# Kernel optimization log

Hardware: AMD Instinct MI355X
Metric: run time of the kernel (lower is better)

## Reference

```python
import jax, jax.numpy as jnp
import numpy as np

BN_EPS = 1e-5
NN_CHUNK = 1024  # unknown points processed per distance-matrix tile


def _batch_ids(cnt, total):
    # contiguous per-batch layout -> batch id of each point via cumsum/searchsorted
    return jnp.searchsorted(jnp.cumsum(cnt), jnp.arange(total), side='right')


def three_nn(unknown, known, ub_id, kb_id):
    """Ragged brute-force 3-NN. Returns (squared dists [N,3], global idx [N,3])."""
    N = unknown.shape[0]
    nchunk = N // NN_CHUNK
    u = unknown.reshape(nchunk, NN_CHUNK, 3)
    ub = ub_id.reshape(nchunk, NN_CHUNK)

    def body(args):
        uc, bc = args
        d2 = jnp.sum((uc[:, None, :] - known[None, :, :]) ** 2, axis=-1)  # [chunk, M]
        d2 = jnp.where(bc[:, None] == kb_id[None, :], d2, jnp.inf)  # mask cross-batch pairs
        neg_d, idx = jax.lax.top_k(-d2, 3)
        return -neg_d, idx

    d2, idx = jax.lax.map(body, (u, ub))
    return d2.reshape(N, 3), idx.reshape(N, 3)


def three_interpolate(known_feats, idx, weight):
    # gather [N,3,C] then inverse-distance weighted sum -> [N,C]
    gathered = known_feats[idx]  # [N,3,C]
    return jnp.einsum('nkc,nk->nc', gathered, weight)


def conv_bn_relu(x, W, gamma, beta):
    # 1x1 Conv2d over [1,C,N,1] == pointwise matmul; BN (training stats) over points
    h = x @ W.T  # [N, C_out]
    mean = jnp.mean(h, axis=0)
    var = jnp.mean((h - mean) ** 2, axis=0)  # biased, as torch BN normalization
    h = (h - mean) * jax.lax.rsqrt(var + BN_EPS) * gamma + beta
    return jax.nn.relu(h)


def setup_inputs() -> dict:
    key = jax.random.key(0)
    ks = jax.random.split(key, 10)
    B, Nper, Mper, C1, C2 = 4, 16384, 4096, 128, 256
    N, M = B * Nper, B * Mper
    unknown = jax.random.normal(ks[0], (N, 3), jnp.float32) * 10.0
    known = jax.random.normal(ks[1], (M, 3), jnp.float32) * 10.0
    unknown_feats = jax.random.normal(ks[2], (N, C1), jnp.float32)
    known_feats = jax.random.normal(ks[3], (M, C2), jnp.float32)
    unknown_batch_cnt = jnp.full((B,), Nper, jnp.int32)
    known_batch_cnt = jnp.full((B,), Mper, jnp.int32)
    Cin = C1 + C2  # 384
    W1 = jax.random.normal(ks[4], (256, Cin), jnp.float32) * (1.0 / np.sqrt(Cin))
    W2 = jax.random.normal(ks[5], (256, 256), jnp.float32) * (1.0 / np.sqrt(256))
    g1 = jnp.ones((256,), jnp.float32); b1 = jnp.zeros((256,), jnp.float32)
    g2 = jnp.ones((256,), jnp.float32); b2 = jnp.zeros((256,), jnp.float32)
    return {"unknown": unknown, "unknown_batch_cnt": unknown_batch_cnt,
            "known": known, "known_batch_cnt": known_batch_cnt,
            "unknown_feats": unknown_feats, "known_feats": known_feats,
            "W1": W1, "g1": g1, "b1": b1, "W2": W2, "g2": g2, "b2": b2}


def reference(unknown, unknown_batch_cnt, known, known_batch_cnt,
              unknown_feats, known_feats, W1, g1, b1, W2, g2, b2):
    ub_id = _batch_ids(unknown_batch_cnt, unknown.shape[0])
    kb_id = _batch_ids(known_batch_cnt, known.shape[0])
    dist, idx = three_nn(unknown, known, ub_id, kb_id)  # squared dists, as CUDA kernel
    dist_recip = 1.0 / (dist + 1e-8)
    weight = dist_recip / jnp.sum(dist_recip, axis=-1, keepdims=True)
    interpolated = three_interpolate(known_feats, idx, weight)  # [N, C2]
    new_features = jnp.concatenate([interpolated, unknown_feats], axis=1)  # [N, C2+C1]
    new_features = conv_bn_relu(new_features, W1, g1, b1)
    new_features = conv_bn_relu(new_features, W2, g2, b2)
    return new_features  # [N, 256]
```

## Files before the change

kernel.cpp:

```cpp
#include <hip/hip_runtime.h>
#include <math.h>

typedef __attribute__((ext_vector_type(8))) short short8;
typedef __attribute__((ext_vector_type(4))) float f32x4;

#define INF 3.0e38f

__device__ __forceinline__ unsigned short f2bf(float x) {
    union { float f; unsigned u; } v; v.f = x;
    unsigned r = v.u + 0x7FFF + ((v.u >> 16) & 1);
    return (unsigned short)(r >> 16);
}

__global__ __launch_bounds__(256) void knn3_kernel(
    const float* __restrict__ unk, const float* __restrict__ kn,
    const int* __restrict__ ucnt, const int* __restrict__ kcnt,
    int B, int N, float* __restrict__ wgt, int* __restrict__ idxo)
{
    __shared__ float md[4][64][3];
    __shared__ float d2g[64];
    __shared__ unsigned long long mk[4][64][3];

    int tid = threadIdx.x;
    int s = __builtin_amdgcn_readfirstlane(tid >> 6);
    int lane = tid & 63;
    int pbase = blockIdx.x * 64;
    int p = pbase + lane;

    int cum = 0, bb = 0;
    for (int i = 0; i < B; i++) { int c = ucnt[i]; if (pbase >= cum) bb = i; cum += c; }
    int kstart = 0;
    for (int i = 0; i < bb; i++) kstart += kcnt[i];
    int kend = kstart + kcnt[bb];

    float ux = unk[p * 3 + 0], uy = unk[p * 3 + 1], uz = unk[p * 3 + 2];

    int qlen = (kend - kstart) >> 2;
    int jbase = kstart + s * qlen;
    const float* kq = kn + (size_t)jbase * 3;

    float d0 = INF, d1 = INF, d2 = INF;
    auto upd = [&](float e) {
        float m0 = fmaxf(e, d0);
        float m1 = fmaxf(e, d1);
        d0 = fminf(e, d0);
        d1 = fminf(m0, d1);
        d2 = fminf(m1, d2);
    };

    for (int i = 0; i < qlen; i += 8) {
        float e[8];
#pragma unroll
        for (int c = 0; c < 8; c++) {
            float kx = kq[(i + c) * 3 + 0];
            float ky = kq[(i + c) * 3 + 1];
            float kz = kq[(i + c) * 3 + 2];
            float dx = kx - ux, dy = ky - uy, dz = kz - uz;
            e[c] = __builtin_fmaf(dx, dx, __builtin_fmaf(dy, dy, dz * dz));
        }
#pragma unroll
        for (int c = 0; c < 8; c++) upd(e[c]);
    }

    md[s][lane][0] = d0; md[s][lane][1] = d1; md[s][lane][2] = d2;
    __syncthreads();
    if (tid < 64) {
        float v0 = INF, v1 = INF, v2 = INF;
#pragma unroll
        for (int w = 0; w < 4; w++)
#pragma unroll
            for (int k = 0; k < 3; k++) {
                float e = md[w][tid][k];
                float m0 = fmaxf(e, v0);
                float m1 = fmaxf(e, v1);
                v0 = fminf(e, v0);
                v1 = fminf(m0, v1);
                v2 = fminf(m1, v2);
            }
        d2g[tid] = v2;
    }
    __syncthreads();
    float thr = d2g[lane];

    unsigned long long s0 = ~0ULL, s1 = ~0ULL, s2 = ~0ULL;
    auto insK = [&](unsigned long long k) {
        bool c0 = k < s0;
        unsigned long long t0 = c0 ? k : s0;
        unsigned long long t1 = c0 ? s0 : k;
        bool c1 = t1 < s1;
        unsigned long long u0 = c1 ? t1 : s1;
        unsigned long long u1 = c1 ? s1 : t1;
        s0 = t0; s1 = u0;
        s2 = u1 < s2 ? u1 : s2;
    };
    auto mkkey = [](float e, int gj) {
        return ((unsigned long long)__float_as_uint(e) << 32) | (unsigned)gj;
    };

    for (int i = 0; i < qlen; i += 4) {
        float e[4];
#pragma unroll
        for (int c = 0; c < 4; c++) {
            float kx = kq[(i + c) * 3 + 0];
            float ky = kq[(i + c) * 3 + 1];
            float kz = kq[(i + c) * 3 + 2];
            float dx = kx - ux, dy = ky - uy, dz = kz - uz;
            e[c] = __builtin_fmaf(dx, dx, __builtin_fmaf(dy, dy, dz * dz));
        }
        float m4 = fminf(fminf(e[0], e[1]), fminf(e[2], e[3]));
        if (m4 <= thr) {
            int gj = jbase + i;
            insK(mkkey(e[0], gj + 0));
            insK(mkkey(e[1], gj + 1));
            insK(mkkey(e[2], gj + 2));
            insK(mkkey(e[3], gj + 3));
        }
    }

    mk[s][lane][0] = s0; mk[s][lane][1] = s1; mk[s][lane][2] = s2;
    __syncthreads();

    if (tid < 64) {
        s0 = s1 = s2 = ~0ULL;
#pragma unroll
        for (int qq = 0; qq < 4; qq++)
#pragma unroll
            for (int kk = 0; kk < 3; kk++)
                insK(mk[qq][tid][kk]);

        float dd0 = __uint_as_float((unsigned)(s0 >> 32));
        float dd1 = __uint_as_float((unsigned)(s1 >> 32));
        float dd2 = __uint_as_float((unsigned)(s2 >> 32));
        float r0 = 1.0f / (dd0 + 1e-8f);
        float r1 = 1.0f / (dd1 + 1e-8f);
        float r2 = 1.0f / (dd2 + 1e-8f);
        float rs = 1.0f / (r0 + r1 + r2);
        int pp = pbase + tid;
        wgt[pp * 3 + 0] = r0 * rs;
        wgt[pp * 3 + 1] = r1 * rs;
        wgt[pp * 3 + 2] = r2 * rs;
        idxo[pp * 3 + 0] = (int)(unsigned)s0;
        idxo[pp * 3 + 1] = (int)(unsigned)s1;
        idxo[pp * 3 + 2] = (int)(unsigned)s2;
    }
}

__global__ __launch_bounds__(256) void build_a1_kernel(
    const float* __restrict__ wgt, const int* __restrict__ idxv,
    const float* __restrict__ kfeat, const float* __restrict__ ufeat,
    unsigned short* __restrict__ A1, int N)
{
    int t = blockIdx.x * 256 + threadIdx.x;
    int p = t >> 6, c4 = t & 63;
    if (p >= N) return;
    float w0 = wgt[p * 3 + 0], w1 = wgt[p * 3 + 1], w2 = wgt[p * 3 + 2];
    int j0 = idxv[p * 3 + 0], j1 = idxv[p * 3 + 1], j2 = idxv[p * 3 + 2];
    float4 v0 = ((const float4*)(kfeat + (size_t)j0 * 256))[c4];
    float4 v1 = ((const float4*)(kfeat + (size_t)j1 * 256))[c4];
    float4 v2 = ((const float4*)(kfeat + (size_t)j2 * 256))[c4];
    ushort4 ob;
    ob.x = f2bf(v0.x * w0 + v1.x * w1 + v2.x * w2);
    ob.y = f2bf(v0.y * w0 + v1.y * w1 + v2.y * w2);
    ob.z = f2bf(v0.z * w0 + v1.z * w1 + v2.z * w2);
    ob.w = f2bf(v0.w * w0 + v1.w * w1 + v2.w * w2);
    *(ushort4*)(A1 + (size_t)p * 384 + c4 * 4) = ob;
    float2 u = ((const float2*)(ufeat + (size_t)p * 128))[c4];
    ushort2 ub; ub.x = f2bf(u.x); ub.y = f2bf(u.y);
    *(ushort2*)(A1 + (size_t)p * 384 + 256 + c4 * 2) = ub;
}

__global__ __launch_bounds__(256) void wconv_kernel(
    const float* __restrict__ W1, const float* __restrict__ W2,
    unsigned short* __restrict__ W1b, unsigned short* __restrict__ W2b,
    int n1, int n2)
{
    int i = blockIdx.x * 256 + threadIdx.x;
    if (i < n1) W1b[i] = f2bf(W1[i]);
    int j = i - n1;
    if (j >= 0 && j < n2) W2b[j] = f2bf(W2[j]);
}

template <int K, int MODE>
__global__ __launch_bounds__(256) void gemm_bf16_kernel(
    const void* __restrict__ Av, const unsigned short* __restrict__ W,
    const float* __restrict__ scale, const float* __restrict__ shift,
    float* __restrict__ C, float* __restrict__ gsum, float* __restrict__ gsq)
{
    __shared__ unsigned short As[128 * 40];
    __shared__ unsigned short Bs[128 * 40];
    __shared__ float colsum[128];
    __shared__ float colsq[128];

    int tid = threadIdx.x;
    int w = tid >> 6, lane = tid & 63;
    int r = w >> 1, cq = w & 1;
    int m16 = lane & 15, q = lane >> 4;
    int bm = blockIdx.x * 128, bn = blockIdx.y * 128;

    f32x4 acc[4][4];
#pragma unroll
    for (int i = 0; i < 4; i++)
#pragma unroll
        for (int j = 0; j < 4; j++) acc[i][j] = (f32x4){0.f, 0.f, 0.f, 0.f};

#pragma unroll
    for (int k0 = 0; k0 < K; k0 += 32) {
        __syncthreads();
#pragma unroll
        for (int i = 0; i < 2; i++) {
            int id = tid + i * 256;
            int row = id >> 2, kc = (id & 3) * 8;
            if (MODE == 0) {
                *(short8*)&As[row * 40 + kc] =
                    *(const short8*)((const unsigned short*)Av +
                                     (size_t)(bm + row) * K + k0 + kc);
            } else {
                const float* Af = (const float*)Av;
                float4 v0 = *(const float4*)(Af + (size_t)(bm + row) * K + k0 + kc);
                float4 v1 = *(const float4*)(Af + (size_t)(bm + row) * K + k0 + kc + 4);
                float4 s0 = *(const float4*)(scale + k0 + kc);
                float4 s1 = *(const float4*)(scale + k0 + kc + 4);
                float4 t0 = *(const float4*)(shift + k0 + kc);
                float4 t1 = *(const float4*)(shift + k0 + kc + 4);
                ushort4 o0, o1;
                o0.x = f2bf(fmaxf(v0.x * s0.x + t0.x, 0.f));
                o0.y = f2bf(fmaxf(v0.y * s0.y + t0.y, 0.f));
                o0.z = f2bf(fmaxf(v0.z * s0.z + t0.z, 0.f));
                o0.w = f2bf(fmaxf(v0.w * s0.w + t0.w, 0.f));
                o1.x = f2bf(fmaxf(v1.x * s1.x + t1.x, 0.f));
                o1.y = f2bf(fmaxf(v1.y * s1.y + t1.y, 0.f));
                o1.z = f2bf(fmaxf(v1.z * s1.z + t1.z, 0.f));
                o1.w = f2bf(fmaxf(v1.w * s1.w + t1.w, 0.f));
                *(ushort4*)&As[row * 40 + kc] = o0;
                *(ushort4*)&As[row * 40 + kc + 4] = o1;
            }
            *(short8*)&Bs[row * 40 + kc] =
                *(const short8*)(W + (size_t)(bn + row) * K + k0 + kc);
        }
        __syncthreads();

        short8 af[4], bf[4];
#pragma unroll
        for (int sub = 0; sub < 4; sub++) {
            af[sub] = *(const short8*)&As[(r * 64 + sub * 16 + m16) * 40 + q * 8];
            bf[sub] = *(const short8*)&Bs[(cq * 64 + sub * 16 + m16) * 40 + q * 8];
        }
#pragma unroll
        for (int sm = 0; sm < 4; sm++)
#pragma unroll
            for (int sn = 0; sn < 4; sn++)
                acc[sm][sn] = __builtin_amdgcn_mfma_f32_16x16x32_bf16(
                    af[sm], bf[sn], acc[sm][sn], 0, 0, 0);
    }

    int row0 = bm + r * 64 + q * 4;
    int col0 = bn + cq * 64 + m16;
#pragma unroll
    for (int sm = 0; sm < 4; sm++)
#pragma unroll
        for (int sn = 0; sn < 4; sn++) {
            f32x4 v = acc[sm][sn];
#pragma unroll
            for (int reg = 0; reg < 4; reg++)
                C[(size_t)(row0 + sm * 16 + reg) * 256 + col0 + sn * 16] = v[reg];
        }

    __syncthreads();
    if (tid < 128) { colsum[tid] = 0.f; colsq[tid] = 0.f; }
    __syncthreads();
#pragma unroll
    for (int sn = 0; sn < 4; sn++) {
        float sacc = 0.f, qacc = 0.f;
#pragma unroll
        for (int sm = 0; sm < 4; sm++) {
            f32x4 v = acc[sm][sn];
#pragma unroll
            for (int reg = 0; reg < 4; reg++) {
                sacc += v[reg];
                qacc += v[reg] * v[reg];
            }
        }
        int lc = cq * 64 + sn * 16 + m16;
        atomicAdd(&colsum[lc], sacc);
        atomicAdd(&colsq[lc], qacc);
    }
    __syncthreads();
    if (tid < 128) {
        atomicAdd(&gsum[bn + tid], colsum[tid]);
        atomicAdd(&gsq[bn + tid], colsq[tid]);
    }
}

__global__ void bn_finalize_kernel(
    const float* __restrict__ sum, const float* __restrict__ sumsq,
    const float* __restrict__ g, const float* __restrict__ bta, float invN,
    float* __restrict__ scale, float* __restrict__ shift)
{
    int c = threadIdx.x;
    float mean = sum[c] * invN;
    float var = sumsq[c] * invN - mean * mean;
    float sc = g[c] * rsqrtf(var + 1e-5f);
    scale[c] = sc;
    shift[c] = bta[c] - mean * sc;
}

__global__ __launch_bounds__(256) void final_act_kernel(
    const float* __restrict__ h2, const float* __restrict__ scale,
    const float* __restrict__ shift, float* __restrict__ out, int total4)
{
    int i = blockIdx.x * 256 + threadIdx.x;
    if (i >= total4) return;
    int c4 = i & 63;
    float4 v = ((const float4*)h2)[i];
    float4 s = ((const float4*)scale)[c4];
    float4 t = ((const float4*)shift)[c4];
    float4 o;
    o.x = fmaxf(v.x * s.x + t.x, 0.0f);
    o.y = fmaxf(v.y * s.y + t.y, 0.0f);
    o.z = fmaxf(v.z * s.z + t.z, 0.0f);
    o.w = fmaxf(v.w * s.w + t.w, 0.0f);
    ((float4*)out)[i] = o;
}

extern "C" void kernel_launch(void* const* d_in, const int* in_sizes, int n_in,
                              void* d_out, int out_size, void* d_ws, size_t ws_size,
                              hipStream_t stream)
{
    const float* unknown = (const float*)d_in[0];
    const int*   ucnt    = (const int*)d_in[1];
    const float* known   = (const float*)d_in[2];
    const int*   kcnt    = (const int*)d_in[3];
    const float* ufeat   = (const float*)d_in[4];
    const float* kfeat   = (const float*)d_in[5];
    const float* W1      = (const float*)d_in[6];
    const float* g1      = (const float*)d_in[7];
    const float* b1      = (const float*)d_in[8];
    const float* W2      = (const float*)d_in[9];
    const float* g2      = (const float*)d_in[10];
    const float* b2      = (const float*)d_in[11];

    int N = in_sizes[0] / 3;
    int B = in_sizes[1];

    char* ws = (char*)d_ws;
    size_t off = 0;
    float* wgt = (float*)(ws + off);            off += (size_t)N * 3 * 4;
    int*   idxb = (int*)(ws + off);             off += (size_t)N * 3 * 4;
    float* stats = (float*)(ws + off);          off += 8 * 256 * 4;
    float* sum1 = stats,         *sq1 = stats + 256;
    float* scale1 = stats + 512, *shift1 = stats + 768;
    float* sum2 = stats + 1024,  *sq2 = stats + 1280;
    float* scale2 = stats + 1536, *shift2 = stats + 1792;
    unsigned short* W1b = (unsigned short*)(ws + off);  off += 256 * 384 * 2;
    unsigned short* W2b = (unsigned short*)(ws + off);  off += 256 * 256 * 2;
    off = (off + 255) & ~(size_t)255;
    unsigned short* A1 = (unsigned short*)(ws + off);
    float* h2 = (float*)(ws + off);
    float* h1 = (float*)d_out;

    hipMemsetAsync(stats, 0, 8 * 256 * 4, stream);

    knn3_kernel<<<N / 64, 256, 0, stream>>>(unknown, known, ucnt, kcnt,
                                            B, N, wgt, idxb);
    wconv_kernel<<<(256 * 384 + 256 * 256 + 255) / 256, 256, 0, stream>>>(
        W1, W2, W1b, W2b, 256 * 384, 256 * 256);
    build_a1_kernel<<<N / 4, 256, 0, stream>>>(wgt, idxb, kfeat, ufeat, A1, N);
    gemm_bf16_kernel<384, 0><<<dim3(N / 128, 2), 256, 0, stream>>>(
        A1, W1b, nullptr, nullptr, h1, sum1, sq1);
    bn_finalize_kernel<<<1, 256, 0, stream>>>(sum1, sq1, g1, b1, 1.0f / N,
                                              scale1, shift1);
    gemm_bf16_kernel<256, 1><<<dim3(N / 128, 2), 256, 0, stream>>>(
        h1, W2b, scale1, shift1, h2, sum2, sq2);
    bn_finalize_kernel<<<1, 256, 0, stream>>>(sum2, sq2, g2, b2, 1.0f / N,
                                              scale2, shift2);
    final_act_kernel<<<N / 4, 256, 0, stream>>>(h2, scale2, shift2,
                                                (float*)d_out, N * 64);
}
```

Measured before the change: 395.5 us.

## Fuse interpolation gather into GEMM1 and BN finalize into consumer kernels

Removes the separate A1-building kernel: the first GEMM now gathers the three neighbour feature rows, applies the interpolation weights and converts to bf16 directly while staging its A tile. It also computes the BN scale and shift per block inside GEMM2 and the final activation kernel, dropping the two single-block finalize launches. The KNN inner loop is unrolled to 8 candidates per threshold check. This saves the A1 write and read round trip and two launches, at the cost of redundant gathers in GEMM1, since each point's neighbour rows are fetched again for both N tiles (blockIdx.y), plus redundant per-block BN stat computation.

```diff
diff --git a/kernel.cpp b/kernel.cpp
--- a/kernel.cpp
+++ b/kernel.cpp
@@ -5,6 +5,7 @@
 typedef __attribute__((ext_vector_type(4))) float f32x4;
 
 #define INF 3.0e38f
+#define BN_EPS 1e-5f
 
 __device__ __forceinline__ unsigned short f2bf(float x) {
     union { float f; unsigned u; } v; v.f = x;
@@ -97,23 +98,22 @@
         return ((unsigned long long)__float_as_uint(e) << 32) | (unsigned)gj;
     };
 
-    for (int i = 0; i < qlen; i += 4) {
-        float e[4];
-#pragma unroll
-        for (int c = 0; c < 4; c++) {
+    for (int i = 0; i < qlen; i += 8) {
+        float e[8];
+#pragma unroll
+        for (int c = 0; c < 8; c++) {
             float kx = kq[(i + c) * 3 + 0];
             float ky = kq[(i + c) * 3 + 1];
             float kz = kq[(i + c) * 3 + 2];
             float dx = kx - ux, dy = ky - uy, dz = kz - uz;
             e[c] = __builtin_fmaf(dx, dx, __builtin_fmaf(dy, dy, dz * dz));
         }
-        float m4 = fminf(fminf(e[0], e[1]), fminf(e[2], e[3]));
-        if (m4 <= thr) {
+        float m8 = fminf(fminf(fminf(e[0], e[1]), fminf(e[2], e[3])),
+                         fminf(fminf(e[4], e[5]), fminf(e[6], e[7])));
+        if (m8 <= thr) {
             int gj = jbase + i;
-            insK(mkkey(e[0], gj + 0));
-            insK(mkkey(e[1], gj + 1));
-            insK(mkkey(e[2], gj + 2));
-            insK(mkkey(e[3], gj + 3));
+#pragma unroll
+            for (int c = 0; c < 8; c++) insK(mkkey(e[c], gj + c));
         }
     }
 
@@ -145,30 +145,6 @@
     }
 }
 
-__global__ __launch_bounds__(256) void build_a1_kernel(
-    const float* __restrict__ wgt, const int* __restrict__ idxv,
-    const float* __restrict__ kfeat, const float* __restrict__ ufeat,
-    unsigned short* __restrict__ A1, int N)
-{
-    int t = blockIdx.x * 256 + threadIdx.x;
-    int p = t >> 6, c4 = t & 63;
-    if (p >= N) return;
-    float w0 = wgt[p * 3 + 0], w1 = wgt[p * 3 + 1], w2 = wgt[p * 3 + 2];
-    int j0 = idxv[p * 3 + 0], j1 = idxv[p * 3 + 1], j2 = idxv[p * 3 + 2];
-    float4 v0 = ((const float4*)(kfeat + (size_t)j0 * 256))[c4];
-    float4 v1 = ((const float4*)(kfeat + (size_t)j1 * 256))[c4];
-    float4 v2 = ((const float4*)(kfeat + (size_t)j2 * 256))[c4];
-    ushort4 ob;
-    ob.x = f2bf(v0.x * w0 + v1.x * w1 + v2.x * w2);
-    ob.y = f2bf(v0.y * w0 + v1.y * w1 + v2.y * w2);
-    ob.z = f2bf(v0.z * w0 + v1.z * w1 + v2.z * w2);
-    ob.w = f2bf(v0.w * w0 + v1.w * w1 + v2.w * w2);
-    *(ushort4*)(A1 + (size_t)p * 384 + c4 * 4) = ob;
-    float2 u = ((const float2*)(ufeat + (size_t)p * 128))[c4];
-    ushort2 ub; ub.x = f2bf(u.x); ub.y = f2bf(u.y);
-    *(ushort2*)(A1 + (size_t)p * 384 + 256 + c4 * 2) = ub;
-}
-
 __global__ __launch_bounds__(256) void wconv_kernel(
     const float* __restrict__ W1, const float* __restrict__ W2,
     unsigned short* __restrict__ W1b, unsigned short* __restrict__ W2b,
@@ -182,14 +158,18 @@
 
 template <int K, int MODE>
 __global__ __launch_bounds__(256) void gemm_bf16_kernel(
-    const void* __restrict__ Av, const unsigned short* __restrict__ W,
-    const float* __restrict__ scale, const float* __restrict__ shift,
+    const void* __restrict__ Aa, const float* __restrict__ ufeat,
+    const unsigned short* __restrict__ W,
+    const float* __restrict__ wgt, const int* __restrict__ idxv,
+    const float* __restrict__ bnsum, const float* __restrict__ bnsq,
+    const float* __restrict__ bng, const float* __restrict__ bnb, float invN,
     float* __restrict__ C, float* __restrict__ gsum, float* __restrict__ gsq)
 {
     __shared__ unsigned short As[128 * 40];
     __shared__ unsigned short Bs[128 * 40];
     __shared__ float colsum[128];
     __shared__ float colsq[128];
+    __shared__ float sc[256], sh[256];
 
     int tid = threadIdx.x;
     int w = tid >> 6, lane = tid & 63;
@@ -197,6 +177,27 @@
     int m16 = lane & 15, q = lane >> 4;
     int bm = blockIdx.x * 128, bn = blockIdx.y * 128;
 
+    if (MODE == 1) {
+        float mean = bnsum[tid] * invN;
+        float var = bnsq[tid] * invN - mean * mean;
+        float scv = bng[tid] * rsqrtf(var + BN_EPS);
+        sc[tid] = scv;
+        sh[tid] = bnb[tid] - mean * scv;
+    }
+
+    int srow = tid >> 2;
+    int kc = (tid & 3) * 8;
+    float w0a[2], w1a[2], w2a[2];
+    int j0a[2], j1a[2], j2a[2];
+    if (MODE == 2) {
+#pragma unroll
+        for (int t = 0; t < 2; t++) {
+            int pp = bm + srow + 64 * t;
+            w0a[t] = wgt[pp * 3 + 0]; w1a[t] = wgt[pp * 3 + 1]; w2a[t] = wgt[pp * 3 + 2];
+            j0a[t] = idxv[pp * 3 + 0]; j1a[t] = idxv[pp * 3 + 1]; j2a[t] = idxv[pp * 3 + 2];
+        }
+    }
+
     f32x4 acc[4][4];
 #pragma unroll
     for (int i = 0; i < 4; i++)
@@ -207,21 +208,45 @@
     for (int k0 = 0; k0 < K; k0 += 32) {
         __syncthreads();
 #pragma unroll
-        for (int i = 0; i < 2; i++) {
-            int id = tid + i * 256;
-            int row = id >> 2, kc = (id & 3) * 8;
-            if (MODE == 0) {
-                *(short8*)&As[row * 40 + kc] =
-                    *(const short8*)((const unsigned short*)Av +
-                                     (size_t)(bm + row) * K + k0 + kc);
+        for (int t = 0; t < 2; t++) {
+            int row = srow + 64 * t;
+            int c = k0 + kc;
+            if (MODE == 2) {
+                ushort4 o0, o1;
+                if (c < 256) {
+                    const float* f0 = (const float*)Aa + (size_t)j0a[t] * 256 + c;
+                    const float* f1 = (const float*)Aa + (size_t)j1a[t] * 256 + c;
+                    const float* f2 = (const float*)Aa + (size_t)j2a[t] * 256 + c;
+                    float4 x0 = *(const float4*)f0, x1 = *(const float4*)(f0 + 4);
+                    float4 y0 = *(const float4*)f1, y1 = *(const float4*)(f1 + 4);
+                    float4 z0 = *(const float4*)f2, z1 = *(const float4*)(f2 + 4);
+                    float W0 = w0a[t], W1 = w1a[t], W2 = w2a[t];
+                    o0.x = f2bf(x0.x * W0 + y0.x * W1 + z0.x * W2);
+                    o0.y = f2bf(x0.y * W0 + y0.y * W1 + z0.y * W2);
+                    o0.z = f2bf(x0.z * W0 + y0.z * W1 + z0.z * W2);
+                    o0.w = f2bf(x0.w * W0 + y0.w * W1 + z0.w * W2);
+                    o1.x = f2bf(x1.x * W0 + y1.x * W1 + z1.x * W2);
+                    o1.y = f2bf(x1.y * W0 + y1.y * W1 + z1.y * W2);
+                    o1.z = f2bf(x1.z * W0 + y1.z * W1 + z1.z * W2);
+                    o1.w = f2bf(x1.w * W0 + y1.w * W1 + z1.w * W2);
+                } else {
+                    const float* fu = ufeat + (size_t)(bm + row) * 128 + (c - 256);
+                    float4 u0 = *(const float4*)fu, u1 = *(const float4*)(fu + 4);
+                    o0.x = f2bf(u0.x); o0.y = f2bf(u0.y);
+                    o0.z = f2bf(u0.z); o0.w = f2bf(u0.w);
+                    o1.x = f2bf(u1.x); o1.y = f2bf(u1.y);
+                    o1.z = f2bf(u1.z); o1.w = f2bf(u1.w);
+                }
+                *(ushort4*)&As[row * 40 + kc] = o0;
+                *(ushort4*)&As[row * 40 + kc + 4] = o1;
             } else {
-                const float* Af = (const float*)Av;
-                float4 v0 = *(const float4*)(Af + (size_t)(bm + row) * K + k0 + kc);
-                float4 v1 = *(const float4*)(Af + (size_t)(bm + row) * K + k0 + kc + 4);
-                float4 s0 = *(const float4*)(scale + k0 + kc);
-                float4 s1 = *(const float4*)(scale + k0 + kc + 4);
-                float4 t0 = *(const float4*)(shift + k0 + kc);
-                float4 t1 = *(const float4*)(shift + k0 + kc + 4);
+                const float* Af = (const float*)Aa;
+                float4 v0 = *(const float4*)(Af + (size_t)(bm + row) * K + c);
+                float4 v1 = *(const float4*)(Af + (size_t)(bm + row) * K + c + 4);
+                float4 s0 = *(const float4*)&sc[c];
+                float4 s1 = *(const float4*)&sc[c + 4];
+                float4 t0 = *(const float4*)&sh[c];
+                float4 t1 = *(const float4*)&sh[c + 4];
                 ushort4 o0, o1;
                 o0.x = f2bf(fmaxf(v0.x * s0.x + t0.x, 0.f));
                 o0.y = f2bf(fmaxf(v0.y * s0.y + t0.y, 0.f));
@@ -291,29 +316,27 @@
     }
 }
 
-__global__ void bn_finalize_kernel(
-    const float* __restrict__ sum, const float* __restrict__ sumsq,
-    const float* __restrict__ g, const float* __restrict__ bta, float invN,
-    float* __restrict__ scale, float* __restrict__ shift)
-{
+__global__ __launch_bounds__(256) void final_act_kernel(
+    const float* __restrict__ h2, const float* __restrict__ bnsum,
+    const float* __restrict__ bnsq, const float* __restrict__ bng,
+    const float* __restrict__ bnb, float invN,
+    float* __restrict__ out, int total4)
+{
+    __shared__ float sc[256], sh[256];
     int c = threadIdx.x;
-    float mean = sum[c] * invN;
-    float var = sumsq[c] * invN - mean * mean;
-    float sc = g[c] * rsqrtf(var + 1e-5f);
-    scale[c] = sc;
-    shift[c] = bta[c] - mean * sc;
-}
-
-__global__ __launch_bounds__(256) void final_act_kernel(
-    const float* __restrict__ h2, const float* __restrict__ scale,
-    const float* __restrict__ shift, float* __restrict__ out, int total4)
-{
+    float mean = bnsum[c] * invN;
+    float var = bnsq[c] * invN - mean * mean;
+    float scv = bng[c] * rsqrtf(var + BN_EPS);
+    sc[c] = scv;
+    sh[c] = bnb[c] - mean * scv;
+    __syncthreads();
+
     int i = blockIdx.x * 256 + threadIdx.x;
     if (i >= total4) return;
     int c4 = i & 63;
     float4 v = ((const float4*)h2)[i];
-    float4 s = ((const float4*)scale)[c4];
-    float4 t = ((const float4*)shift)[c4];
+    float4 s = *(const float4*)&sc[c4 * 4];
+    float4 t = *(const float4*)&sh[c4 * 4];
     float4 o;
     o.x = fmaxf(v.x * s.x + t.x, 0.0f);
     o.y = fmaxf(v.y * s.y + t.y, 0.0f);
@@ -346,33 +369,29 @@
     size_t off = 0;
     float* wgt = (float*)(ws + off);            off += (size_t)N * 3 * 4;
     int*   idxb = (int*)(ws + off);             off += (size_t)N * 3 * 4;
-    float* stats = (float*)(ws + off);          off += 8 * 256 * 4;
-    float* sum1 = stats,         *sq1 = stats + 256;
-    float* scale1 = stats + 512, *shift1 = stats + 768;
-    float* sum2 = stats + 1024,  *sq2 = stats + 1280;
-    float* scale2 = stats + 1536, *shift2 = stats + 1792;
+    float* stats = (float*)(ws + off);          off += 4 * 256 * 4;
+    float* sum1 = stats,        *sq1 = stats + 256;
+    float* sum2 = stats + 512,  *sq2 = stats + 768;
     unsigned short* W1b = (unsigned short*)(ws + off);  off += 256 * 384 * 2;
     unsigned short* W2b = (unsigned short*)(ws + off);  off += 256 * 256 * 2;
     off = (off + 255) & ~(size_t)255;
-    unsigned short* A1 = (unsigned short*)(ws + off);
     float* h2 = (float*)(ws + off);
     float* h1 = (float*)d_out;
 
-    hipMemsetAsync(stats, 0, 8 * 256 * 4, stream);
+    float invN = 1.0f / (float)N;
+
+    hipMemsetAsync(stats, 0, 4 * 256 * 4, stream);
 
     knn3_kernel<<<N / 64, 256, 0, stream>>>(unknown, known, ucnt, kcnt,
                                             B, N, wgt, idxb);
     wconv_kernel<<<(256 * 384 + 256 * 256 + 255) / 256, 256, 0, stream>>>(
         W1, W2, W1b, W2b, 256 * 384, 256 * 256);
-    build_a1_kernel<<<N / 4, 256, 0, stream>>>(wgt, idxb, kfeat, ufeat, A1, N);
-    gemm_bf16_kernel<384, 0><<<dim3(N / 128, 2), 256, 0, stream>>>(
-        A1, W1b, nullptr, nullptr, h1, sum1, sq1);
-    bn_finalize_kernel<<<1, 256, 0, stream>>>(sum1, sq1, g1, b1, 1.0f / N,
-                                              scale1, shift1);
+    gemm_bf16_kernel<384, 2><<<dim3(N / 128, 2), 256, 0, stream>>>(
+        kfeat, ufeat, W1b, wgt, idxb,
+        nullptr, nullptr, nullptr, nullptr, 0.f, h1, sum1, sq1);
     gemm_bf16_kernel<256, 1><<<dim3(N / 128, 2), 256, 0, stream>>>(
-        h1, W2b, scale1, shift1, h2, sum2, sq2);
-    bn_finalize_kernel<<<1, 256, 0, stream>>>(sum2, sq2, g2, b2, 1.0f / N,
-                                              scale2, shift2);
-    final_act_kernel<<<N / 4, 256, 0, stream>>>(h2, scale2, shift2,
+        h1, nullptr, W2b, nullptr, nullptr,
+        sum1, sq1, g1, b1, invN, h2, sum2, sq2);
+    final_act_kernel<<<N / 4, 256, 0, stream>>>(h2, sum2, sq2, g2, b2, invN,
                                                 (float*)d_out, N * 64);
 }
```

Measured after the change: 399.1 us. Within noise of the previous version (+0.9%).
